# Kernel tuning notes

Measured on AMD Instinct MI355X. Metric: run time of the kernel, lower is better.

## Reference

```python
import jax, jax.numpy as jnp
import numpy as np

EPS = 1e-6

def _ln(x, g, b):
    mu = x.mean(-1, keepdims=True)
    var = ((x - mu) ** 2).mean(-1, keepdims=True)
    return (x - mu) * jax.lax.rsqrt(var + EPS) * g + b

def _ln_l2_grad(z, target, g, b):
    # grad of 0.5*||LN(z)*g+b - target||^2 wrt z (fused L2/LayerNorm backward used by TTT)
    d = z.shape[-1]
    mu = z.mean(-1, keepdims=True)
    var = ((z - mu) ** 2).mean(-1, keepdims=True)
    std = jnp.sqrt(var + EPS)
    zh = (z - mu) / std
    go = (zh * g + b) - target
    gxh = go * g
    return (d * gxh - gxh.sum(-1, keepdims=True) - zh * (gxh * zh).sum(-1, keepdims=True)) / (d * std)

def _forward(x, W_down, b_down, Wq, Wk, Wv, Wo, W1, b1, ttt_g, ttt_b,
             lr_w, lr_b, post_g, post_b, norm_g, norm_b, W_up, b_up):
    B, S, D = x.shape
    A = W_down.shape[1]
    H, hd, _ = W1.shape
    # adapter down projection + SiLU
    h = jax.nn.silu(x @ W_down + b_down)                      # [B,S,A]
    # TTT-Linear: q/k/v projections split into heads
    xq = (h @ Wq).reshape(B, S, H, hd)
    xk = (h @ Wk).reshape(B, S, H, hd)
    xv = (h @ Wv).reshape(B, S, H, hd)
    eta = jax.nn.sigmoid(h @ lr_w + lr_b) / hd                # [B,S,H] token-wise learnable inner lr (base_lr=1)
    W1_0 = jnp.broadcast_to(W1, (B, H, hd, hd))
    b1_0 = jnp.broadcast_to(b1, (B, H, 1, hd))
    xs = (xq.transpose(1, 0, 2, 3), xk.transpose(1, 0, 2, 3),
          xv.transpose(1, 0, 2, 3), eta.transpose(1, 0, 2))

    def step(carry, ins):
        W, bb = carry                                         # [B,H,hd,hd], [B,H,1,hd]
        q, k, v, e = ins                                      # [B,H,hd] x3, [B,H]
        Z = jnp.einsum('bhd,bhde->bhe', k, W) + bb[:, :, 0, :]
        g = _ln_l2_grad(Z, v - k, ttt_g, ttt_b)               # inner-loop grad wrt pre-LN activations
        e4 = e[:, :, None, None]
        Wn = W - e4 * (k[..., :, None] * g[..., None, :])     # fast-weight SGD update
        bn = bb - e4 * g[:, :, None, :]
        Zq = jnp.einsum('bhd,bhde->bhe', q, Wn) + bn[:, :, 0, :]
        out = q + _ln(Zq, ttt_g, ttt_b)                       # per-head TTT post residual
        return (Wn, bn), out

    _, ys = jax.lax.scan(step, (W1_0, b1_0), xs)              # ys: [S,B,H,hd]
    t = ys.transpose(1, 0, 2, 3).reshape(B, S, A)
    t = _ln(t, post_g, post_b) @ Wo                           # TTT post-norm + output projection
    out = _ln(t, norm_g, norm_b)                              # adapter LayerNorm
    return out @ W_up + b_up                                  # adapter up projection (residual unused in source)

def setup_inputs() -> dict:
    key = jax.random.key(0)
    ks = jax.random.split(key, 12)
    B, S, D, A, H = 4, 1024, 768, 192, 3
    hd = A // H
    s = 0.02
    return {
        'x': jax.random.normal(ks[0], (B, S, D), jnp.float32),
        'W_down': jax.random.normal(ks[1], (D, A), jnp.float32) * s,
        'b_down': jnp.zeros((A,), jnp.float32),
        'Wq': jax.random.normal(ks[2], (A, A), jnp.float32) * s,
        'Wk': jax.random.normal(ks[3], (A, A), jnp.float32) * s,
        'Wv': jax.random.normal(ks[4], (A, A), jnp.float32) * s,
        'Wo': jax.random.normal(ks[5], (A, A), jnp.float32) * s,
        'W1': jax.random.normal(ks[6], (H, hd, hd), jnp.float32) * s,
        'b1': jnp.zeros((H, 1, hd), jnp.float32),
        'ttt_g': jnp.ones((H, hd), jnp.float32),
        'ttt_b': jnp.zeros((H, hd), jnp.float32),
        'lr_w': jax.random.normal(ks[7], (A, H), jnp.float32) * s,
        'lr_b': jnp.zeros((H,), jnp.float32),
        'post_g': jnp.ones((A,), jnp.float32),
        'post_b': jnp.zeros((A,), jnp.float32),
        'norm_g': jnp.ones((A,), jnp.float32),
        'norm_b': jnp.zeros((A,), jnp.float32),
        'W_up': jax.random.normal(ks[8], (A, D), jnp.float32) * s,
        'b_up': jnp.zeros((D,), jnp.float32),
    }

def reference(x, W_down, b_down, Wq, Wk, Wv, Wo, W1, b1, ttt_g, ttt_b,
              lr_w, lr_b, post_g, post_b, norm_g, norm_b, W_up, b_up):
    return _forward(x, W_down, b_down, Wq, Wk, Wv, Wo, W1, b1, ttt_g, ttt_b,
                    lr_w, lr_b, post_g, post_b, norm_g, norm_b, W_up, b_up)
```

## Files before the change

### kernel.cpp

```cpp
#include <hip/hip_runtime.h>
#include <hip/hip_bf16.h>
#include <math.h>

#define BDIM 4
#define SDIM 1024
#define DDIM 768
#define ADIM 192
#define HDIM 3
#define HD   64
#define MROWS (BDIM*SDIM)
#define NCHUNK (SDIM/32)
#define EPSLN 1e-6f

template<int CTRL, int RMASK, bool BC>
__device__ __forceinline__ float dpp_add_step(float x) {
    int t = __builtin_amdgcn_update_dpp(0, __float_as_int(x), CTRL, RMASK, 0xf, BC);
    return x + __int_as_float(t);
}
__device__ __forceinline__ float wave_bcast_sum(float x) {
    x = dpp_add_step<0x111, 0xf, true >(x);
    x = dpp_add_step<0x112, 0xf, true >(x);
    x = dpp_add_step<0x114, 0xf, true >(x);
    x = dpp_add_step<0x118, 0xf, true >(x);
    x = dpp_add_step<0x142, 0xa, false>(x);
    x = dpp_add_step<0x143, 0xc, false>(x);
    return __int_as_float(__builtin_amdgcn_readlane(__float_as_int(x), 63));
}
__device__ __forceinline__ float rl(float v, int lane) {
    return __int_as_float(__builtin_amdgcn_readlane(__float_as_int(v), lane));
}
__device__ __forceinline__ float fast_rsq(float x) {
    float r;
    asm("v_rsq_f32 %0, %1" : "=v"(r) : "v"(x));
    return r;
}
__device__ __forceinline__ void red5_asm(float& a, float& b, float& c,
                                         float& d, float& e) {
#define R5_SHR(N)                                                              \
    asm("v_add_f32 %0, %0, %0 row_shr:" #N " row_mask:0xf bank_mask:0xf bound_ctrl:0" : "+v"(a)); \
    asm("v_add_f32 %0, %0, %0 row_shr:" #N " row_mask:0xf bank_mask:0xf bound_ctrl:0" : "+v"(b)); \
    asm("v_add_f32 %0, %0, %0 row_shr:" #N " row_mask:0xf bank_mask:0xf bound_ctrl:0" : "+v"(c)); \
    asm("v_add_f32 %0, %0, %0 row_shr:" #N " row_mask:0xf bank_mask:0xf bound_ctrl:0" : "+v"(d)); \
    asm("v_add_f32 %0, %0, %0 row_shr:" #N " row_mask:0xf bank_mask:0xf bound_ctrl:0" : "+v"(e));
#define R5_BC(N, RM)                                                           \
    asm("v_add_f32 %0, %0, %0 row_bcast:" #N " row_mask:" #RM " bank_mask:0xf" : "+v"(a)); \
    asm("v_add_f32 %0, %0, %0 row_bcast:" #N " row_mask:" #RM " bank_mask:0xf" : "+v"(b)); \
    asm("v_add_f32 %0, %0, %0 row_bcast:" #N " row_mask:" #RM " bank_mask:0xf" : "+v"(c)); \
    asm("v_add_f32 %0, %0, %0 row_bcast:" #N " row_mask:" #RM " bank_mask:0xf" : "+v"(d)); \
    asm("v_add_f32 %0, %0, %0 row_bcast:" #N " row_mask:" #RM " bank_mask:0xf" : "+v"(e));
    R5_SHR(1) R5_SHR(2) R5_SHR(4) R5_SHR(8)
    R5_BC(15, 0xa) R5_BC(31, 0xc)
#undef R5_SHR
#undef R5_BC
}

__global__ __launch_bounds__(64) void lnstats(
    const float* __restrict__ in, float2* __restrict__ st)
{
    int row = blockIdx.x, tid = threadIdx.x;
    float x0 = in[(size_t)row * ADIM + tid];
    float x1 = in[(size_t)row * ADIM + 64 + tid];
    float x2 = in[(size_t)row * ADIM + 128 + tid];
    float s1 = wave_bcast_sum((x0 + x1) + x2);
    float s2 = wave_bcast_sum(fmaf(x0, x0, fmaf(x1, x1, x2 * x2)));
    if (tid == 0) {
        float mu = s1 * (1.f / 192.f);
        float var = s2 * (1.f / 192.f) - mu * mu;
        st[row] = make_float2(mu, rsqrtf(var + EPSLN));
    }
}

template<int ACT, int LAYOUT, int LNA>
__global__ __launch_bounds__(256) void gemm_k(
    const float* __restrict__ A, const float* __restrict__ Bm,
    const float* __restrict__ bias, float* __restrict__ C,
    int M, int N, int K,
    const float2* __restrict__ lnst, const float* __restrict__ lng,
    const float* __restrict__ lnbb)
{
    __shared__ float As[16][68];
    __shared__ float Bs[16][68];
    const int tid = threadIdx.x;
    const int bm = blockIdx.y * 64, bn = blockIdx.x * 64;
    const int tr = tid >> 4, tc = tid & 15;
    float acc[4][4] = {};

    for (int k0 = 0; k0 < K; k0 += 16) {
        #pragma unroll
        for (int p = 0; p < 4; ++p) {
            int m = (tid >> 4) + p * 16;
            int kk = tid & 15;
            float av = A[(size_t)(bm + m) * K + k0 + kk];
            if (LNA) {
                float2 stv = lnst[bm + m];
                av = fmaf((av - stv.x) * stv.y, lng[k0 + kk], lnbb[k0 + kk]);
            }
            As[kk][m] = av;
        }
        #pragma unroll
        for (int p = 0; p < 4; ++p) {
            int kk = (tid >> 6) + p * 4;
            int n = tid & 63;
            Bs[kk][n] = Bm[(size_t)(k0 + kk) * N + bn + n];
        }
        __syncthreads();
        #pragma unroll
        for (int kk = 0; kk < 16; ++kk) {
            const float4 a4 = *(const float4*)&As[kk][tr * 4];
            const float4 b4 = *(const float4*)&Bs[kk][tc * 4];
            float aa[4] = {a4.x, a4.y, a4.z, a4.w};
            float bb[4] = {b4.x, b4.y, b4.z, b4.w};
            #pragma unroll
            for (int i = 0; i < 4; ++i)
                #pragma unroll
                for (int j = 0; j < 4; ++j)
                    acc[i][j] = fmaf(aa[i], bb[j], acc[i][j]);
        }
        __syncthreads();
    }

    #pragma unroll
    for (int i = 0; i < 4; ++i) {
        int m = bm + tr * 4 + i;
        #pragma unroll
        for (int j = 0; j < 4; ++j) {
            int n = bn + tc * 4 + j;
            float v = acc[i][j];
            if (bias) v += bias[n];
            if (ACT == 1) v = v / (1.f + __expf(-v));
            if (LAYOUT == 0) {
                C[(size_t)m * N + n] = v;
            } else {
                int b  = m >> 10, s = m & 1023;
                int hh = n >> 6,  d = n & 63;
                C[(((size_t)b * HDIM + hh) * SDIM + s) * HD + d] = v;
            }
        }
    }
}

__global__ __launch_bounds__(256) void gemm_qkv(
    const float* __restrict__ A, const float* __restrict__ BWq,
    const float* __restrict__ BWk, const float* __restrict__ BWv,
    float* __restrict__ Cbase)
{
    const float* Bm = (blockIdx.z == 0) ? BWq : (blockIdx.z == 1) ? BWk : BWv;
    float* C = Cbase + (size_t)blockIdx.z * ((size_t)MROWS * ADIM);
    __shared__ float As[16][68];
    __shared__ float Bs[16][68];
    const int tid = threadIdx.x;
    const int bm = blockIdx.y * 64, bn = blockIdx.x * 64;
    const int tr = tid >> 4, tc = tid & 15;
    float acc[4][4] = {};

    for (int k0 = 0; k0 < ADIM; k0 += 16) {
        #pragma unroll
        for (int p = 0; p < 4; ++p) {
            int m = (tid >> 4) + p * 16;
            int kk = tid & 15;
            As[kk][m] = A[(size_t)(bm + m) * ADIM + k0 + kk];
        }
        #pragma unroll
        for (int p = 0; p < 4; ++p) {
            int kk = (tid >> 6) + p * 4;
            int n = tid & 63;
            Bs[kk][n] = Bm[(size_t)(k0 + kk) * ADIM + bn + n];
        }
        __syncthreads();
        #pragma unroll
        for (int kk = 0; kk < 16; ++kk) {
            const float4 a4 = *(const float4*)&As[kk][tr * 4];
            const float4 b4 = *(const float4*)&Bs[kk][tc * 4];
            float aa[4] = {a4.x, a4.y, a4.z, a4.w};
            float bb[4] = {b4.x, b4.y, b4.z, b4.w};
            #pragma unroll
            for (int i = 0; i < 4; ++i)
                #pragma unroll
                for (int j = 0; j < 4; ++j)
                    acc[i][j] = fmaf(aa[i], bb[j], acc[i][j]);
        }
        __syncthreads();
    }

    #pragma unroll
    for (int i = 0; i < 4; ++i) {
        int m = bm + tr * 4 + i;
        #pragma unroll
        for (int j = 0; j < 4; ++j) {
            int n = bn + tc * 4 + j;
            int b  = m >> 10, s = m & 1023;
            int hh = n >> 6,  d = n & 63;
            C[(((size_t)b * HDIM + hh) * SDIM + s) * HD + d] = acc[i][j];
        }
    }
}

__global__ __launch_bounds__(192) void eta_kernel(
    const float* __restrict__ h, const float* __restrict__ lr_w,
    const float* __restrict__ lr_b, float* __restrict__ etab)
{
    const int row = blockIdx.x, tid = threadIdx.x, wave = tid >> 6;
    __shared__ float part[3][3];
    float hv = h[(size_t)row * ADIM + tid];
    float p0 = hv * lr_w[tid * 3 + 0];
    float p1 = hv * lr_w[tid * 3 + 1];
    float p2 = hv * lr_w[tid * 3 + 2];
    float s0 = wave_bcast_sum(p0);
    float s1 = wave_bcast_sum(p1);
    float s2 = wave_bcast_sum(p2);
    if ((tid & 63) == 0) {
        part[wave][0] = s0; part[wave][1] = s1; part[wave][2] = s2;
    }
    __syncthreads();
    if (tid < 3) {
        float acc = (part[0][tid] + part[1][tid]) + part[2][tid] + lr_b[tid];
        float e = 1.f / (1.f + __expf(-acc)) * (1.f / 64.f);
        int b = row >> 10, s = row & 1023;
        etab[((size_t)(b * HDIM + tid)) * SDIM + s] = e;
    }
}

__global__ __launch_bounds__(256) void ab_kernel(
    const float* __restrict__ qb, const float* __restrict__ kb,
    float* __restrict__ vb,
    const float* __restrict__ ttt_g, const float* __restrict__ ttt_b,
    float* __restrict__ Ab, float* __restrict__ Bb,
    float* __restrict__ r6b)
{
    int bh = blockIdx.x >> 5, c = blockIdx.x & 31, cs = c * 32;
    int hh = bh % HDIM;
    __shared__ float Kc[32][65], Qc[32][65], Vc[32][65];
    for (int i = threadIdx.x; i < 2048; i += 256) {
        int t = i >> 6, j = i & 63;
        Kc[t][j] = kb[((size_t)bh * SDIM + cs + t) * HD + j];
        Qc[t][j] = qb[((size_t)bh * SDIM + cs + t) * HD + j];
        Vc[t][j] = vb[((size_t)bh * SDIM + cs + t) * HD + j];
    }
    __syncthreads();
    size_t base = ((size_t)(bh * NCHUNK + c)) * 1024;
    for (int e = threadIdx.x; e < 1024; e += 256) {
        int t = e >> 5, s = e & 31;
        float a = 1.f, b = 1.f;
        #pragma unroll
        for (int j = 0; j < 64; ++j) {
            float ks = Kc[s][j];
            a = fmaf(Kc[t][j], ks, a);
            b = fmaf(Qc[t][j], ks, b);
        }
        Ab[base + e] = a;
        Bb[base + e] = b;
    }
    for (int i = threadIdx.x; i < 2048; i += 256) {
        int t = i >> 6, j = i & 63;
        float gwv = ttt_g[hh * 64 + j], bwv = ttt_b[hh * 64 + j];
        float av = fmaf(-(Vc[t][j] - Kc[t][j]), gwv, bwv * gwv);
        Vc[t][j] = av;
        vb[((size_t)bh * SDIM + cs + t) * HD + j] = av;
    }
    __syncthreads();
    if (threadIdx.x < 32) {
        int t = threadIdx.x;
        float acc = 0.f;
        #pragma unroll
        for (int j = 0; j < 64; ++j) acc += Vc[t][j];
        r6b[(size_t)bh * SDIM + cs + t] = acc;
    }
}

__device__ __forceinline__ void stage_chunk(
    int pp, int cc, int bh, int idx, int nth,
    const float* __restrict__ kbuf, const float* __restrict__ abuf,
    const float* __restrict__ Ab, const float* __restrict__ etab,
    const float* __restrict__ r6b,
    float4* K4, float4* a4, float4* A4, float2* er6)
{
    const float4* kg = (const float4*)(kbuf + ((size_t)bh * SDIM + cc * 32) * HD);
    const float4* ag = (const float4*)(abuf + ((size_t)bh * SDIM + cc * 32) * HD);
    const float4* Ag = (const float4*)(Ab + ((size_t)(bh * NCHUNK + cc)) * 1024);
    for (int i = idx; i < 512; i += nth) K4[pp * 512 + i] = kg[i];
    for (int i = idx; i < 512; i += nth) a4[pp * 512 + i] = ag[i];
    for (int i = idx; i < 256; i += nth) A4[pp * 256 + i] = Ag[i];
    for (int i = idx; i < 32; i += nth)
        er6[pp * 32 + i] = make_float2(
            etab[(size_t)bh * SDIM + cc * 32 + i] * (1.f / 64.f),
            r6b[(size_t)bh * SDIM + cc * 32 + i]);
}

__global__ __launch_bounds__(256, 1) void ttt_scan(
    const float* __restrict__ kbuf, const float* __restrict__ abuf,
    const float* __restrict__ etab, const float* __restrict__ Ab,
    const float* __restrict__ r6b,
    const float* __restrict__ W1,   const float* __restrict__ b1,
    const float* __restrict__ ttt_g, const float* __restrict__ ttt_b,
    float* __restrict__ Gbuf, float* __restrict__ W0save, float* __restrict__ b0save)
{
    const int bh = blockIdx.x, hh = bh % HDIM;
    const int tid = threadIdx.x, lane = tid & 63;
    const int wv = tid >> 6;
    __shared__ float  Zp[4][16][64];
    __shared__ float4 K4s[2 * 512];
    __shared__ float4 a4s[2 * 512];
    __shared__ float4 A4s[2 * 256];
    __shared__ float2 er6s[2 * 32];
    __shared__ float  Gl[16][64];

    float Wreg[16];
    #pragma unroll
    for (int r = 0; r < 16; ++r)
        Wreg[r] = W1[hh * 4096 + (wv * 16 + r) * 64 + lane];
    float breg = b1[hh * 64 + lane];
    const float gw = ttt_g[hh * 64 + lane];
    const float bw = ttt_b[hh * 64 + lane];
    const float w3 = gw * gw;
    (void)bw;
    const float Cg2 = wave_bcast_sum(w3);
    const float* a_f = (const float*)a4s;

    stage_chunk(0, 0, bh, tid, 256, kbuf, abuf, Ab, etab, r6b,
                K4s, a4s, A4s, er6s);
    __syncthreads();

    for (int c = 0; c < NCHUNK; ++c) {
        const int cs = c * 32;
        const int p = c & 1;

        {
            float* Wd = W0save + ((size_t)(bh * NCHUNK + c)) * 4096
                        + (wv * 16) * 64 + lane;
            #pragma unroll
            for (int r = 0; r < 16; ++r) Wd[r * 64] = Wreg[r];
            if (tid < 64) b0save[(bh * NCHUNK + c) * 64 + tid] = breg;
        }

        #pragma unroll
        for (int h = 0; h < 2; ++h) {
            const int h16 = h * 16, h4 = h * 4;

            float Zt[16];
            #pragma unroll
            for (int i = 0; i < 16; ++i) {
                const int t = h16 + i;
                float zt = 0.f;
                #pragma unroll
                for (int r4 = 0; r4 < 4; ++r4) {
                    const float4 kv = K4s[p * 512 + t * 16 + wv * 4 + r4];
                    zt = fmaf(kv.x, Wreg[r4 * 4 + 0], zt);
                    zt = fmaf(kv.y, Wreg[r4 * 4 + 1], zt);
                    zt = fmaf(kv.z, Wreg[r4 * 4 + 2], zt);
                    zt = fmaf(kv.w, Wreg[r4 * 4 + 3], zt);
                }
                Zt[i] = zt;
            }
            if (wv != 0) {
                #pragma unroll
                for (int i = 0; i < 16; ++i)
                    Zp[wv][i][lane] = (wv == 1) ? Zt[i] + breg : Zt[i];
            }
            __syncthreads();

            if (wv == 0) {
                __builtin_amdgcn_s_setprio(1);
                float Z[16];
                #pragma unroll
                for (int i = 0; i < 16; ++i) {
                    float q1 = Zp[1][i][lane], q2 = Zp[2][i][lane],
                          q3 = Zp[3][i][lane];
                    Z[i] = ((Zt[i] + q1) + (q2 + q3));
                }
                float4 avA[4], avB[4];
                float aA, aB; float2 erA, erB;
                #pragma unroll
                for (int q = 0; q < 4; ++q)
                    avA[q] = A4s[p * 256 + h16 * 8 + h4 + q];
                aA  = a_f[p * 2048 + h16 * 64 + lane];
                erA = er6s[p * 32 + h16];
#define TOK(I, avC, aC, erC, avN, aN, erN)                                     \
    {                                                                          \
        if ((I) < 15) {                                                        \
            _Pragma("unroll")                                                  \
            for (int q = ((I) + 2) >> 2; q < 4; ++q)                           \
                avN[q] = A4s[p * 256 + (h16 + (I) + 1) * 8 + h4 + q];          \
            aN  = a_f[p * 2048 + (h16 + (I) + 1) * 64 + lane];                 \
            erN = er6s[p * 32 + h16 + (I) + 1];                                \
        }                                                                      \
        float z  = Z[I];                                                       \
        float a  = aC;                                                         \
        float zg = z * w3;                                                     \
        float x1 = z, x2 = z * z, x3 = zg, x4 = zg * z, x5 = z * a;            \
        red5_asm(x1, x2, x3, x4, x5);                                          \
        float r1 = rl(x1, 63), r2 = rl(x2, 63), r3 = rl(x3, 63);               \
        float r4 = rl(x4, 63), r5 = rl(x5, 63);                                \
        float r6t = (erC).y;                                                   \
        float mu   = r1 * (1.f / 64.f);                                        \
        float var  = fmaf(-mu, mu, r2 * (1.f / 64.f));                         \
        float rstd = fast_rsq(var + EPSLN);                                    \
        float mc   = mu * Cg2;                                                 \
        float sgxh = fmaf(rstd, r3 - mc, r6t);                                 \
        float t4v  = fmaf(mu, mc, fmaf(-2.f * mu, r3, r4));                    \
        float sgz  = fmaf(rstd * rstd, t4v, rstd * (r5 - mu * r6t));           \
        float zh   = (z - mu) * rstd;                                          \
        float gxh  = fmaf(zh, w3, a);                                          \
        float ge   = (fmaf(64.f, gxh, -sgxh) - zh * sgz) * (rstd * (erC).x);   \
        Gl[I][lane] = ge;                                                      \
        _Pragma("unroll")                                                      \
        for (int u = (I) + 1; u < 16; ++u) {                                   \
            const float4 c4 = avC[(u) >> 2]; const int m4 = (u) & 3;           \
            float Atu = (m4 == 0) ? c4.x : (m4 == 1) ? c4.y                    \
                      : (m4 == 2) ? c4.z : c4.w;                               \
            Z[u] = fmaf(-Atu, ge, Z[u]);                                       \
        }                                                                      \
    }
                #pragma unroll
                for (int tp = 0; tp < 8; ++tp) {
                    TOK(2 * tp,     avA, aA, erA, avB, aB, erB)
                    TOK(2 * tp + 1, avB, aB, erB, avA, aA, erA)
                }
#undef TOK
                __builtin_amdgcn_s_setprio(0);
            } else if (h == 0 && c < NCHUNK - 1) {
                stage_chunk(p ^ 1, c + 1, bh, tid - 64, 192,
                            kbuf, abuf, Ab, etab, r6b, K4s, a4s, A4s, er6s);
            }
            __syncthreads();

            float btot = 0.f;
            #pragma unroll
            for (int s = 0; s < 16; ++s) {
                float gd = Gl[s][lane];
                btot += gd;
                #pragma unroll
                for (int r4 = 0; r4 < 4; ++r4) {
                    const float4 kv = K4s[p * 512 + (h16 + s) * 16 + wv * 4 + r4];
                    Wreg[r4 * 4 + 0] = fmaf(-kv.x, gd, Wreg[r4 * 4 + 0]);
                    Wreg[r4 * 4 + 1] = fmaf(-kv.y, gd, Wreg[r4 * 4 + 1]);
                    Wreg[r4 * 4 + 2] = fmaf(-kv.z, gd, Wreg[r4 * 4 + 2]);
                    Wreg[r4 * 4 + 3] = fmaf(-kv.w, gd, Wreg[r4 * 4 + 3]);
                }
            }
            breg -= btot;
            {
                float* gb = Gbuf + ((size_t)bh * SDIM + cs + h16) * HD + lane;
                #pragma unroll
                for (int r = 0; r < 4; ++r)
                    gb[(wv * 4 + r) * HD] = Gl[wv * 4 + r][lane];
            }
        }
    }
}

__global__ __launch_bounds__(256) void post_kernel(
    const float* __restrict__ qbuf, const float* __restrict__ Bb,
    const float* __restrict__ Gbuf, const float* __restrict__ W0save,
    const float* __restrict__ b0save,
    const float* __restrict__ ttt_g, const float* __restrict__ ttt_b,
    float* __restrict__ ys)
{
    const int bh = blockIdx.x >> 5, c = blockIdx.x & 31, cs = c * 32;
    const int b = bh / HDIM, hh = bh % HDIM;
    const int tid = threadIdx.x, lane = tid & 63, wave = tid >> 6;
    __shared__ float Qc[32][65];
    __shared__ float W0l[64][65];
    __shared__ float Gl[32][64];
    for (int i = tid; i < 2048; i += 256) {
        int t = i >> 6, j = i & 63;
        Qc[t][j] = qbuf[((size_t)bh * SDIM + cs + t) * HD + j];
        Gl[t][j] = Gbuf[((size_t)bh * SDIM + cs + t) * HD + j];
    }
    for (int i = tid; i < 4096; i += 256)
        W0l[i >> 6][i & 63] = W0save[((size_t)(bh * NCHUNK + c)) * 4096 + i];
    __syncthreads();

    const float bb0 = b0save[(bh * NCHUNK + c) * 64 + lane];
    const float gw = ttt_g[hh * 64 + lane], bw = ttt_b[hh * 64 + lane];
    float acc[8];
    #pragma unroll
    for (int r = 0; r < 8; ++r) acc[r] = bb0;
    for (int j = 0; j < 64; ++j) {
        float w0 = W0l[j][lane];
        #pragma unroll
        for (int r = 0; r < 8; ++r)
            acc[r] = fmaf(Qc[wave * 8 + r][j], w0, acc[r]);
    }
    float Breg[8];
    size_t bbase = ((size_t)(bh * NCHUNK + c)) * 1024;
    #pragma unroll
    for (int r = 0; r < 8; ++r)
        Breg[r] = Bb[bbase + (wave * 8 + r) * 32 + (lane & 31)];
    #pragma unroll
    for (int s = 0; s < 32; ++s) {
        float gd = Gl[s][lane];
        #pragma unroll
        for (int r = 0; r < 8; ++r) {
            int t = wave * 8 + r;
            float Bts = rl(Breg[r], s);
            acc[r] = (s <= t) ? fmaf(-Bts, gd, acc[r]) : acc[r];
        }
    }
    #pragma unroll
    for (int r = 0; r < 8; ++r) {
        int t = wave * 8 + r;
        float s1 = wave_bcast_sum(acc[r]);
        float s2 = wave_bcast_sum(acc[r] * acc[r]);
        float mu = s1 * (1.f / 64.f);
        float var = s2 * (1.f / 64.f) - mu * mu;
        float rstd = rsqrtf(var + EPSLN);
        float zh = (acc[r] - mu) * rstd;
        float val = zh * gw + bw + Qc[t][lane];
        ys[((size_t)(b * SDIM) + cs + t) * ADIM + hh * HD + lane] = val;
    }
}

extern "C" void kernel_launch(void* const* d_in, const int* in_sizes, int n_in,
                              void* d_out, int out_size, void* d_ws, size_t ws_size,
                              hipStream_t stream)
{
    const float* x      = (const float*)d_in[0];
    const float* W_down = (const float*)d_in[1];
    const float* b_down = (const float*)d_in[2];
    const float* Wq     = (const float*)d_in[3];
    const float* Wk     = (const float*)d_in[4];
    const float* Wv     = (const float*)d_in[5];
    const float* Wo     = (const float*)d_in[6];
    const float* W1     = (const float*)d_in[7];
    const float* b1     = (const float*)d_in[8];
    const float* ttt_g  = (const float*)d_in[9];
    const float* ttt_b  = (const float*)d_in[10];
    const float* lr_w   = (const float*)d_in[11];
    const float* lr_b   = (const float*)d_in[12];
    const float* post_g = (const float*)d_in[13];
    const float* post_b = (const float*)d_in[14];
    const float* norm_g = (const float*)d_in[15];
    const float* norm_b = (const float*)d_in[16];
    const float* W_up   = (const float*)d_in[17];
    const float* b_up   = (const float*)d_in[18];
    float* out = (float*)d_out;

    float* ws = (float*)d_ws;
    const size_t SZ = (size_t)MROWS * ADIM;
    float* h    = ws;
    float* qb   = ws + SZ;
    float* kb   = ws + 2 * SZ;
    float* vb   = ws + 3 * SZ;
    float* Gb   = ws + 4 * SZ;
    float* etab = ws + 5 * SZ;
    float* Ab   = etab + 12288;
    float* Bb   = Ab + 393216;
    float* W0s  = Bb + 393216;
    float* b0s  = W0s + 1572864;
    float* r6b  = b0s + 24576;
    float2* lnst = (float2*)(r6b + 12288);
    float* ysb  = h;
    float* tbuf = qb;

    gemm_k<1, 0, 0><<<dim3(ADIM / 64, MROWS / 64), 256, 0, stream>>>(
        x, W_down, b_down, h, MROWS, ADIM, DDIM, nullptr, nullptr, nullptr);
    gemm_qkv<<<dim3(ADIM / 64, MROWS / 64, 3), 256, 0, stream>>>(
        h, Wq, Wk, Wv, qb);
    eta_kernel<<<MROWS, 192, 0, stream>>>(h, lr_w, lr_b, etab);
    ab_kernel<<<BDIM * HDIM * NCHUNK, 256, 0, stream>>>(
        qb, kb, vb, ttt_g, ttt_b, Ab, Bb, r6b);
    ttt_scan<<<BDIM * HDIM, 256, 0, stream>>>(
        kb, vb, etab, Ab, r6b, W1, b1, ttt_g, ttt_b, Gb, W0s, b0s);
    post_kernel<<<BDIM * HDIM * NCHUNK, 256, 0, stream>>>(
        qb, Bb, Gb, W0s, b0s, ttt_g, ttt_b, ysb);
    lnstats<<<MROWS, 64, 0, stream>>>(ysb, lnst);
    gemm_k<0, 0, 1><<<dim3(ADIM / 64, MROWS / 64), 256, 0, stream>>>(
        ysb, Wo, nullptr, tbuf, MROWS, ADIM, ADIM, lnst, post_g, post_b);
    lnstats<<<MROWS, 64, 0, stream>>>(tbuf, lnst);
    gemm_k<0, 0, 1><<<dim3(DDIM / 64, MROWS / 64), 256, 0, stream>>>(
        tbuf, W_up, b_up, out, MROWS, DDIM, ADIM, lnst, norm_g, norm_b);
}
```

Before: 462.6 us.

## Fuse LayerNorm stats into producer epilogues and eta into ab_kernel

```diff
diff --git a/kernel.cpp b/kernel.cpp
--- a/kernel.cpp
+++ b/kernel.cpp
@@ -25,6 +25,13 @@
     x = dpp_add_step<0x142, 0xa, false>(x);
     x = dpp_add_step<0x143, 0xc, false>(x);
     return __int_as_float(__builtin_amdgcn_readlane(__float_as_int(x), 63));
+}
+__device__ __forceinline__ float dpp_row16_sum(float x) {
+    x = dpp_add_step<0x111, 0xf, true >(x);
+    x = dpp_add_step<0x112, 0xf, true >(x);
+    x = dpp_add_step<0x114, 0xf, true >(x);
+    x = dpp_add_step<0x118, 0xf, true >(x);
+    return x;
 }
 __device__ __forceinline__ float rl(float v, int lane) {
     return __int_as_float(__builtin_amdgcn_readlane(__float_as_int(v), lane));
@@ -54,45 +61,40 @@
 #undef R5_BC
 }
 
-__global__ __launch_bounds__(64) void lnstats(
-    const float* __restrict__ in, float2* __restrict__ st)
-{
-    int row = blockIdx.x, tid = threadIdx.x;
-    float x0 = in[(size_t)row * ADIM + tid];
-    float x1 = in[(size_t)row * ADIM + 64 + tid];
-    float x2 = in[(size_t)row * ADIM + 128 + tid];
-    float s1 = wave_bcast_sum((x0 + x1) + x2);
-    float s2 = wave_bcast_sum(fmaf(x0, x0, fmaf(x1, x1, x2 * x2)));
-    if (tid == 0) {
-        float mu = s1 * (1.f / 192.f);
-        float var = s2 * (1.f / 192.f) - mu * mu;
-        st[row] = make_float2(mu, rsqrtf(var + EPSLN));
-    }
-}
-
-template<int ACT, int LAYOUT, int LNA>
+template<int ACT, int LAYOUT, int LNA, int STATS>
 __global__ __launch_bounds__(256) void gemm_k(
     const float* __restrict__ A, const float* __restrict__ Bm,
     const float* __restrict__ bias, float* __restrict__ C,
     int M, int N, int K,
     const float2* __restrict__ lnst, const float* __restrict__ lng,
-    const float* __restrict__ lnbb)
+    const float* __restrict__ lnbb, float2* __restrict__ ostat)
 {
     __shared__ float As[16][68];
     __shared__ float Bs[16][68];
+    __shared__ float2 lst[64];
     const int tid = threadIdx.x;
     const int bm = blockIdx.y * 64, bn = blockIdx.x * 64;
     const int tr = tid >> 4, tc = tid & 15;
     float acc[4][4] = {};
 
+    if (LNA == 2) {
+        if (tid < 64) {
+            float2 s = lnst[bm + tid];
+            float mu = s.x * (1.f / 192.f);
+            float var = fmaf(-mu, mu, s.y * (1.f / 192.f));
+            lst[tid] = make_float2(mu, rsqrtf(var + EPSLN));
+        }
+        __syncthreads();
+    }
+
     for (int k0 = 0; k0 < K; k0 += 16) {
         #pragma unroll
         for (int p = 0; p < 4; ++p) {
             int m = (tid >> 4) + p * 16;
             int kk = tid & 15;
             float av = A[(size_t)(bm + m) * K + k0 + kk];
-            if (LNA) {
-                float2 stv = lnst[bm + m];
+            if (LNA == 2) {
+                float2 stv = lst[m];
                 av = fmaf((av - stv.x) * stv.y, lng[k0 + kk], lnbb[k0 + kk]);
             }
             As[kk][m] = av;
@@ -119,6 +121,7 @@
         __syncthreads();
     }
 
+    float rs1[4] = {}, rs2[4] = {};
     #pragma unroll
     for (int i = 0; i < 4; ++i) {
         int m = bm + tr * 4 + i;
@@ -128,12 +131,27 @@
             float v = acc[i][j];
             if (bias) v += bias[n];
             if (ACT == 1) v = v / (1.f + __expf(-v));
+            if (STATS) { rs1[i] += v; rs2[i] = fmaf(v, v, rs2[i]); }
             if (LAYOUT == 0) {
                 C[(size_t)m * N + n] = v;
             } else {
                 int b  = m >> 10, s = m & 1023;
                 int hh = n >> 6,  d = n & 63;
                 C[(((size_t)b * HDIM + hh) * SDIM + s) * HD + d] = v;
+            }
+        }
+    }
+    if (STATS) {
+        #pragma unroll
+        for (int i = 0; i < 4; ++i) {
+            rs1[i] = dpp_row16_sum(rs1[i]);
+            rs2[i] = dpp_row16_sum(rs2[i]);
+        }
+        if (tc == 15) {
+            #pragma unroll
+            for (int i = 0; i < 4; ++i) {
+                atomicAdd(&ostat[bm + tr * 4 + i].x, rs1[i]);
+                atomicAdd(&ostat[bm + tr * 4 + i].y, rs2[i]);
             }
         }
     }
@@ -195,41 +213,36 @@
     }
 }
 
-__global__ __launch_bounds__(192) void eta_kernel(
-    const float* __restrict__ h, const float* __restrict__ lr_w,
-    const float* __restrict__ lr_b, float* __restrict__ etab)
-{
-    const int row = blockIdx.x, tid = threadIdx.x, wave = tid >> 6;
-    __shared__ float part[3][3];
-    float hv = h[(size_t)row * ADIM + tid];
-    float p0 = hv * lr_w[tid * 3 + 0];
-    float p1 = hv * lr_w[tid * 3 + 1];
-    float p2 = hv * lr_w[tid * 3 + 2];
-    float s0 = wave_bcast_sum(p0);
-    float s1 = wave_bcast_sum(p1);
-    float s2 = wave_bcast_sum(p2);
-    if ((tid & 63) == 0) {
-        part[wave][0] = s0; part[wave][1] = s1; part[wave][2] = s2;
-    }
-    __syncthreads();
-    if (tid < 3) {
-        float acc = (part[0][tid] + part[1][tid]) + part[2][tid] + lr_b[tid];
-        float e = 1.f / (1.f + __expf(-acc)) * (1.f / 64.f);
-        int b = row >> 10, s = row & 1023;
-        etab[((size_t)(b * HDIM + tid)) * SDIM + s] = e;
-    }
-}
-
 __global__ __launch_bounds__(256) void ab_kernel(
     const float* __restrict__ qb, const float* __restrict__ kb,
     float* __restrict__ vb,
     const float* __restrict__ ttt_g, const float* __restrict__ ttt_b,
     float* __restrict__ Ab, float* __restrict__ Bb,
-    float* __restrict__ r6b)
+    float* __restrict__ r6b,
+    const float* __restrict__ h, const float* __restrict__ lr_w,
+    const float* __restrict__ lr_b, float* __restrict__ etab,
+    float4* __restrict__ stz)
 {
     int bh = blockIdx.x >> 5, c = blockIdx.x & 31, cs = c * 32;
-    int hh = bh % HDIM;
+    int hh = bh % HDIM, b = bh / HDIM;
     __shared__ float Kc[32][65], Qc[32][65], Vc[32][65];
+    __shared__ float ep[32][8];
+
+    if (blockIdx.x < 16) {
+        float4 z4; z4.x = z4.y = z4.z = z4.w = 0.f;
+        stz[blockIdx.x * 256 + threadIdx.x] = z4;
+    }
+
+    {
+        int rg = threadIdx.x >> 3, sl = threadIdx.x & 7;
+        const float* hrow = h + ((size_t)b * SDIM + cs + rg) * ADIM + sl * 24;
+        float esum = 0.f;
+        #pragma unroll
+        for (int jj = 0; jj < 24; ++jj)
+            esum = fmaf(hrow[jj], lr_w[(sl * 24 + jj) * 3 + hh], esum);
+        ep[rg][sl] = esum;
+    }
+
     for (int i = threadIdx.x; i < 2048; i += 256) {
         int t = i >> 6, j = i & 63;
         Kc[t][j] = kb[((size_t)bh * SDIM + cs + t) * HD + j];
@@ -237,18 +250,28 @@
         Vc[t][j] = vb[((size_t)bh * SDIM + cs + t) * HD + j];
     }
     __syncthreads();
+
+    if (threadIdx.x < 32) {
+        int t = threadIdx.x;
+        float acc = ((ep[t][0] + ep[t][1]) + (ep[t][2] + ep[t][3]))
+                  + ((ep[t][4] + ep[t][5]) + (ep[t][6] + ep[t][7]))
+                  + lr_b[hh];
+        float e = 1.f / (1.f + __expf(-acc)) * (1.f / 64.f);
+        etab[(size_t)bh * SDIM + cs + t] = e;
+    }
+
     size_t base = ((size_t)(bh * NCHUNK + c)) * 1024;
     for (int e = threadIdx.x; e < 1024; e += 256) {
         int t = e >> 5, s = e & 31;
-        float a = 1.f, b = 1.f;
+        float a = 1.f, bv = 1.f;
         #pragma unroll
         for (int j = 0; j < 64; ++j) {
             float ks = Kc[s][j];
-            a = fmaf(Kc[t][j], ks, a);
-            b = fmaf(Qc[t][j], ks, b);
+            a  = fmaf(Kc[t][j], ks, a);
+            bv = fmaf(Qc[t][j], ks, bv);
         }
         Ab[base + e] = a;
-        Bb[base + e] = b;
+        Bb[base + e] = bv;
     }
     for (int i = threadIdx.x; i < 2048; i += 256) {
         int t = i >> 6, j = i & 63;
@@ -453,7 +476,7 @@
     const float* __restrict__ Gbuf, const float* __restrict__ W0save,
     const float* __restrict__ b0save,
     const float* __restrict__ ttt_g, const float* __restrict__ ttt_b,
-    float* __restrict__ ys)
+    float* __restrict__ ys, float2* __restrict__ ystat)
 {
     const int bh = blockIdx.x >> 5, c = blockIdx.x & 31, cs = c * 32;
     const int b = bh / HDIM, hh = bh % HDIM;
@@ -507,6 +530,12 @@
         float zh = (acc[r] - mu) * rstd;
         float val = zh * gw + bw + Qc[t][lane];
         ys[((size_t)(b * SDIM) + cs + t) * ADIM + hh * HD + lane] = val;
+        float t1 = wave_bcast_sum(val);
+        float t2 = wave_bcast_sum(val * val);
+        if (lane == 0) {
+            atomicAdd(&ystat[(size_t)b * SDIM + cs + t].x, t1);
+            atomicAdd(&ystat[(size_t)b * SDIM + cs + t].y, t2);
+        }
     }
 }
 
@@ -548,25 +577,27 @@
     float* W0s  = Bb + 393216;
     float* b0s  = W0s + 1572864;
     float* r6b  = b0s + 24576;
-    float2* lnst = (float2*)(r6b + 12288);
+    float2* ystat = (float2*)(r6b + 12288);
+    float2* tstat = ystat + 4096;
     float* ysb  = h;
     float* tbuf = qb;
 
-    gemm_k<1, 0, 0><<<dim3(ADIM / 64, MROWS / 64), 256, 0, stream>>>(
-        x, W_down, b_down, h, MROWS, ADIM, DDIM, nullptr, nullptr, nullptr);
+    gemm_k<1, 0, 0, 0><<<dim3(ADIM / 64, MROWS / 64), 256, 0, stream>>>(
+        x, W_down, b_down, h, MROWS, ADIM, DDIM,
+        nullptr, nullptr, nullptr, nullptr);
     gemm_qkv<<<dim3(ADIM / 64, MROWS / 64, 3), 256, 0, stream>>>(
         h, Wq, Wk, Wv, qb);
-    eta_kernel<<<MROWS, 192, 0, stream>>>(h, lr_w, lr_b, etab);
     ab_kernel<<<BDIM * HDIM * NCHUNK, 256, 0, stream>>>(
-        qb, kb, vb, ttt_g, ttt_b, Ab, Bb, r6b);
+        qb, kb, vb, ttt_g, ttt_b, Ab, Bb, r6b,
+        h, lr_w, lr_b, etab, (float4*)ystat);
     ttt_scan<<<BDIM * HDIM, 256, 0, stream>>>(
         kb, vb, etab, Ab, r6b, W1, b1, ttt_g, ttt_b, Gb, W0s, b0s);
     post_kernel<<<BDIM * HDIM * NCHUNK, 256, 0, stream>>>(
-        qb, Bb, Gb, W0s, b0s, ttt_g, ttt_b, ysb);
-    lnstats<<<MROWS, 64, 0, stream>>>(ysb, lnst);
-    gemm_k<0, 0, 1><<<dim3(ADIM / 64, MROWS / 64), 256, 0, stream>>>(
-        ysb, Wo, nullptr, tbuf, MROWS, ADIM, ADIM, lnst, post_g, post_b);
-    lnstats<<<MROWS, 64, 0, stream>>>(tbuf, lnst);
-    gemm_k<0, 0, 1><<<dim3(DDIM / 64, MROWS / 64), 256, 0, stream>>>(
-        tbuf, W_up, b_up, out, MROWS, DDIM, ADIM, lnst, norm_g, norm_b);
-}
+        qb, Bb, Gb, W0s, b0s, ttt_g, ttt_b, ysb, ystat);
+    gemm_k<0, 0, 2, 1><<<dim3(ADIM / 64, MROWS / 64), 256, 0, stream>>>(
+        ysb, Wo, nullptr, tbuf, MROWS, ADIM, ADIM,
+        ystat, post_g, post_b, tstat);
+    gemm_k<0, 0, 2, 0><<<dim3(DDIM / 64, MROWS / 64), 256, 0, stream>>>(
+        tbuf, W_up, b_up, out, MROWS, DDIM, ADIM,
+        tstat, norm_g, norm_b, nullptr);
+}
```

Result: no change. 455.3 us (-1.6%).
